# Optimization experiments

Hardware: AMD Instinct MI355X
Metric: run time of the kernel (lower is better)

The kernel has to match this reference:

```python
import jax, jax.numpy as jnp
import numpy as np

BN_EPS = 1e-5


def setup_inputs() -> dict:
    key = jax.random.key(0)
    k1, k2, k3 = jax.random.split(key, 3)
    B, C, N = 8, 64, 4096
    x = jax.random.normal(k1, (B, C, N, 1), dtype=jnp.float32)
    w = jax.random.normal(k2, (B, N), dtype=jnp.float32)
    conv_w = jax.random.normal(k3, (C, C, 1, 1), dtype=jnp.float32) * (1.0 / np.sqrt(C))
    conv_b = jnp.zeros((C,), dtype=jnp.float32)
    bn_gamma = jnp.ones((C,), dtype=jnp.float32)
    bn_beta = jnp.zeros((C,), dtype=jnp.float32)
    return {"x": x, "w": w, "conv_w": conv_w, "conv_b": conv_b,
            "bn_gamma": bn_gamma, "bn_beta": bn_beta}


def _graph_aggregation(x, w):
    # x: [B, C, N, 1], w: [B, N]
    B, C, N, _ = x.shape
    wv = jax.nn.relu(jnp.tanh(w))                       # [B, N]
    # torch.bmm(w^T, w) with w [B,N,1] -> [B,1,1] inner product (faithful)
    s = jnp.sum(wv * wv, axis=-1)[:, None, None]        # [B, 1, 1]
    A = s + jnp.eye(N, dtype=x.dtype)                   # broadcast -> [B, N, N]
    d = jnp.sum(A, axis=-1)                             # [B, N]
    dinv = (1.0 / d) ** 0.5                             # [B, N]
    # diag(D) @ A @ diag(D) == row/col scaling (same math, no diag materialize)
    L = dinv[:, :, None] * A * dinv[:, None, :]         # [B, N, N]
    L = jax.lax.stop_gradient(L)                        # torch.no_grad block
    feat = jnp.transpose(x[..., 0], (0, 2, 1))          # [B, N, C]
    out = jnp.einsum('bnm,bmc->bnc', L, feat)           # [B, N, C]
    return jnp.transpose(out, (0, 2, 1))[..., None]     # [B, C, N, 1]


def reference(x, w, conv_w, conv_b, bn_gamma, bn_beta):
    out = _graph_aggregation(x, w)                      # [B, C, N, 1]
    # 1x1 conv == channel matmul
    y = jnp.einsum('oc,bcnk->bonk', conv_w[:, :, 0, 0], out) + conv_b[None, :, None, None]
    # BatchNorm2d (training-mode forward: batch statistics over B,N,1)
    mean = jnp.mean(y, axis=(0, 2, 3), keepdims=True)
    var = jnp.var(y, axis=(0, 2, 3), keepdims=True)
    yhat = (y - mean) * jax.lax.rsqrt(var + BN_EPS)
    y = yhat * bn_gamma[None, :, None, None] + bn_beta[None, :, None, None]
    return jax.nn.relu(y)
```

## Files before the change

kernel.cpp:

```cpp
#include <hip/hip_runtime.h>
#include <math.h>

#define B_ 8
#define C_ 64
#define N_ 4096
#define NT_ 32

#define GP_OFF  0
#define CSP_OFF (NT_ * B_ * C_ * C_)
#define G_OFF   (CSP_OFF + NT_ * B_ * C_)
#define CS_OFF  (G_OFF + B_ * C_ * C_)
#define SS_OFF  (CS_OFF + B_ * C_)
#define SC_OFF  (SS_OFF + B_)
#define A_OFF   (SC_OFF + B_)
#define BB_OFF  (A_OFF + B_ * C_)

__global__ __launch_bounds__(256) void k_gram(const float* __restrict__ x,
                                              const float* __restrict__ wvec,
                                              float* __restrict__ ws) {
    const int b = blockIdx.y;
    const int t = threadIdx.x;

    __shared__ float xs[128 * 65];

    if (blockIdx.x == NT_) {
        const float4* wb = reinterpret_cast<const float4*>(wvec + (size_t)b * N_);
        float p = 0.f;
        #pragma unroll
        for (int i = 0; i < 4; ++i) {
            const float4 v = wb[t + i * 256];
            const float vv[4] = {v.x, v.y, v.z, v.w};
            #pragma unroll
            for (int j = 0; j < 4; ++j)
                if (vv[j] > 0.f) { const float th = tanhf(vv[j]); p += th * th; }
        }
        #pragma unroll
        for (int m = 32; m >= 1; m >>= 1) p += __shfl_xor(p, m);
        if ((t & 63) == 0) xs[t >> 6] = p;
        __syncthreads();
        if (t == 0) {
            const float s = xs[0] + xs[1] + xs[2] + xs[3];
            ws[SS_OFF + b] = s;
            ws[SC_OFF + b] = 1.f / ((float)N_ * s + 1.f);
        }
        return;
    }

    const int tile = blockIdx.x;
    const float* xb = x + (size_t)b * C_ * N_ + (size_t)tile * 128;

    const int k0 = (t & 31) * 4;
    float csum[8];
    #pragma unroll
    for (int it = 0; it < 8; ++it) {
        const int cc = it * 8 + (t >> 5);
        const float4 v = *reinterpret_cast<const float4*>(xb + (size_t)cc * N_ + k0);
        xs[(k0 + 0) * 65 + cc] = v.x;
        xs[(k0 + 1) * 65 + cc] = v.y;
        xs[(k0 + 2) * 65 + cc] = v.z;
        xs[(k0 + 3) * 65 + cc] = v.w;
        csum[it] = v.x + v.y + v.z + v.w;
    }
    __syncthreads();

    const int c1 = (t >> 4) * 4;
    const int c2 = (t & 15) * 4;
    float acc[4][4] = {};
    for (int k = 0; k < 128; ++k) {
        const float* row = &xs[k * 65];
        const float a0 = row[c1 + 0], a1 = row[c1 + 1], a2 = row[c1 + 2], a3 = row[c1 + 3];
        const float b0 = row[c2 + 0], b1 = row[c2 + 1], b2 = row[c2 + 2], b3 = row[c2 + 3];
        acc[0][0] += a0 * b0; acc[0][1] += a0 * b1; acc[0][2] += a0 * b2; acc[0][3] += a0 * b3;
        acc[1][0] += a1 * b0; acc[1][1] += a1 * b1; acc[1][2] += a1 * b2; acc[1][3] += a1 * b3;
        acc[2][0] += a2 * b0; acc[2][1] += a2 * b1; acc[2][2] += a2 * b2; acc[2][3] += a2 * b3;
        acc[3][0] += a3 * b0; acc[3][1] += a3 * b1; acc[3][2] += a3 * b2; acc[3][3] += a3 * b3;
    }

    #pragma unroll
    for (int it = 0; it < 8; ++it) {
        float s4 = csum[it];
        #pragma unroll
        for (int m = 16; m >= 1; m >>= 1) s4 += __shfl_xor(s4, m, 32);
        if ((t & 31) == 0)
            ws[CSP_OFF + (tile * B_ + b) * C_ + it * 8 + (t >> 5)] = s4;
    }

    float* Gp = ws + GP_OFF + (size_t)(tile * B_ + b) * (C_ * C_);
    #pragma unroll
    for (int i = 0; i < 4; ++i) {
        float4 r;
        r.x = acc[i][0]; r.y = acc[i][1]; r.z = acc[i][2]; r.w = acc[i][3];
        *reinterpret_cast<float4*>(&Gp[(c1 + i) * 64 + c2]) = r;
    }
}

__global__ __launch_bounds__(256) void k_reduce(float* __restrict__ ws) {
    const int blk = blockIdx.x;
    const int b = blk >> 3, slice = blk & 7;
    const int t = threadIdx.x;

    #pragma unroll
    for (int h = 0; h < 2; ++h) {
        const int e = h * 256 + t;
        const int c = slice * 8 + (e >> 6);
        const int cc = e & 63;
        float s = 0.f;
        #pragma unroll 8
        for (int p = 0; p < NT_; ++p)
            s += ws[GP_OFF + (size_t)(p * B_ + b) * (C_ * C_) + c * 64 + cc];
        ws[G_OFF + (size_t)b * (C_ * C_) + c * 64 + cc] = s;
    }
    if (slice == 0 && t < 64) {
        float s = 0.f;
        #pragma unroll 8
        for (int p = 0; p < NT_; ++p)
            s += ws[CSP_OFF + (p * B_ + b) * C_ + t];
        ws[CS_OFF + b * 64 + t] = s;
    }
}

__global__ __launch_bounds__(256) void k_finalize(const float* __restrict__ conv_w,
                                                  const float* __restrict__ conv_b,
                                                  const float* __restrict__ gamma,
                                                  const float* __restrict__ beta,
                                                  float* __restrict__ ws) {
    const int o = blockIdx.x;
    const int t = threadIdx.x;

    __shared__ float Wrow[64];
    __shared__ float Tq[8], Qq[8];

    if (t < 64) Wrow[t] = conv_w[o * 64 + t];
    __syncthreads();

    float pT[2], pQ[2];
    #pragma unroll
    for (int h = 0; h < 2; ++h) {
        const int r = t + h * 256;
        const int bb = r >> 6, c = r & 63;
        const float* Grow = ws + G_OFF + ((size_t)(bb * 64 + c)) * 64;
        float dot = 0.f;
        #pragma unroll 8
        for (int cc = 0; cc < 64; ++cc) dot += Wrow[cc] * Grow[cc];
        pQ[h] = Wrow[c] * dot;
        pT[h] = Wrow[c] * ws[CS_OFF + bb * 64 + c];
    }
    #pragma unroll
    for (int m = 32; m >= 1; m >>= 1) {
        pQ[0] += __shfl_xor(pQ[0], m);
        pQ[1] += __shfl_xor(pQ[1], m);
        pT[0] += __shfl_xor(pT[0], m);
        pT[1] += __shfl_xor(pT[1], m);
    }
    if ((t & 63) == 0) {
        const int wv = t >> 6;
        Tq[wv] = pT[0]; Qq[wv] = pQ[0];
        Tq[wv + 4] = pT[1]; Qq[wv + 4] = pQ[1];
    }
    __syncthreads();

    if (t == 0) {
        float Sy = 0.f, Syy = 0.f;
        float qv[8];
        #pragma unroll
        for (int b = 0; b < 8; ++b) {
            const float sS = ws[SS_OFF + b];
            const float sc = ws[SC_OFF + b];
            const float T  = sc * Tq[b];
            const float q  = sS * T + conv_b[o];
            qv[b] = q;
            Sy  += T + 4096.f * q;
            Syy += sc * sc * Qq[b] + 2.f * q * T + 4096.f * q * q;
        }
        const float mean  = Sy / 32768.f;
        const float var   = Syy / 32768.f - mean * mean;
        const float alpha = gamma[o] * rsqrtf(var + 1e-5f);
        #pragma unroll
        for (int b = 0; b < 8; ++b) {
            ws[A_OFF  + b * 64 + o] = ws[SC_OFF + b] * alpha;
            ws[BB_OFF + b * 64 + o] = (qv[b] - mean) * alpha + beta[o];
        }
    }
}

__global__ __launch_bounds__(512) void k_main(const float* __restrict__ x,
                                              const float* __restrict__ conv_w,
                                              const float* __restrict__ ws,
                                              float* __restrict__ out) {
    const int nt = blockIdx.x;
    const int b  = blockIdx.y;
    const int t  = threadIdx.x;

    __shared__ float xsm[64 * 128];

    const int n0 = nt * 128;
    const float* xb = x + (size_t)b * C_ * N_ + n0;

    const int k0 = (t & 31) * 4;
    #pragma unroll
    for (int it = 0; it < 4; ++it) {
        const int cc = it * 16 + (t >> 5);
        *reinterpret_cast<float4*>(&xsm[cc * 128 + k0]) =
            *reinterpret_cast<const float4*>(xb + (size_t)cc * N_ + k0);
    }

    const int o0 = __builtin_amdgcn_readfirstlane((t >> 6) * 8);
    const int nn = (t & 63) * 2;

    float au[8], bu[8];
    #pragma unroll
    for (int i = 0; i < 8; ++i) {
        au[i] = ws[A_OFF  + b * 64 + o0 + i];
        bu[i] = ws[BB_OFF + b * 64 + o0 + i];
    }
    __syncthreads();

    float acc[8][2] = {};
    #pragma unroll 4
    for (int c = 0; c < 64; ++c) {
        const float2 xv = *reinterpret_cast<const float2*>(&xsm[c * 128 + nn]);
        #pragma unroll
        for (int i = 0; i < 8; ++i) {
            const float wv = conv_w[(o0 + i) * 64 + c];
            acc[i][0] += wv * xv.x;
            acc[i][1] += wv * xv.y;
        }
    }

    #pragma unroll
    for (int i = 0; i < 8; ++i) {
        float2 r;
        r.x = fmaxf(acc[i][0] * au[i] + bu[i], 0.f);
        r.y = fmaxf(acc[i][1] * au[i] + bu[i], 0.f);
        *reinterpret_cast<float2*>(out + ((size_t)(b * 64 + o0 + i)) * N_ + n0 + nn) = r;
    }
}

extern "C" void kernel_launch(void* const* d_in, const int* in_sizes, int n_in,
                              void* d_out, int out_size, void* d_ws, size_t ws_size,
                              hipStream_t stream) {
    (void)in_sizes; (void)n_in; (void)out_size; (void)ws_size;
    const float* x      = (const float*)d_in[0];
    const float* w      = (const float*)d_in[1];
    const float* conv_w = (const float*)d_in[2];
    const float* conv_b = (const float*)d_in[3];
    const float* gamma  = (const float*)d_in[4];
    const float* beta   = (const float*)d_in[5];
    float* out = (float*)d_out;
    float* ws  = (float*)d_ws;

    k_gram<<<dim3(NT_ + 1, B_), 256, 0, stream>>>(x, w, ws);
    k_reduce<<<64, 256, 0, stream>>>(ws);
    k_finalize<<<64, 256, 0, stream>>>(conv_w, conv_b, gamma, beta, ws);
    k_main<<<dim3(32, B_), 512, 0, stream>>>(x, conv_w, ws, out);
}
```

Baseline: 103.3 us.

## Replace Gram-matrix statistics with direct conv output and per-tile moment sums

Instead of computing per-batch channel Gram matrices to derive BatchNorm statistics analytically, the conv output W·x is computed once, stored to workspace, and its per-channel sum and sum of squares are reduced per tile. A single-block stats kernel folds these into per-(batch,channel) scale and shift. An elementwise kernel then applies the affine transform and ReLU. This drops the Gram GEMM, its partial-sum reduction and the second read of x, and cuts four launches to three. In exchange it adds a write and re-read of a full-size intermediate tensor.

```diff
diff --git a/kernel.cpp b/kernel.cpp
--- a/kernel.cpp
+++ b/kernel.cpp
@@ -6,29 +6,29 @@
 #define N_ 4096
 #define NT_ 32
 
-#define GP_OFF  0
-#define CSP_OFF (NT_ * B_ * C_ * C_)
-#define G_OFF   (CSP_OFF + NT_ * B_ * C_)
-#define CS_OFF  (G_OFF + B_ * C_ * C_)
-#define SS_OFF  (CS_OFF + B_ * C_)
+#define M_OFF   0
+#define SMP_OFF (B_ * C_ * N_)
+#define SQP_OFF (SMP_OFF + NT_ * B_ * C_)
+#define SS_OFF  (SQP_OFF + NT_ * B_ * C_)
 #define SC_OFF  (SS_OFF + B_)
 #define A_OFF   (SC_OFF + B_)
 #define BB_OFF  (A_OFF + B_ * C_)
 
-__global__ __launch_bounds__(256) void k_gram(const float* __restrict__ x,
+__global__ __launch_bounds__(512) void k_conv(const float* __restrict__ x,
                                               const float* __restrict__ wvec,
+                                              const float* __restrict__ conv_w,
                                               float* __restrict__ ws) {
     const int b = blockIdx.y;
     const int t = threadIdx.x;
 
-    __shared__ float xs[128 * 65];
+    __shared__ float xsm[64 * 128];
 
     if (blockIdx.x == NT_) {
         const float4* wb = reinterpret_cast<const float4*>(wvec + (size_t)b * N_);
         float p = 0.f;
         #pragma unroll
-        for (int i = 0; i < 4; ++i) {
-            const float4 v = wb[t + i * 256];
+        for (int i = 0; i < 2; ++i) {
+            const float4 v = wb[t + i * 512];
             const float vv[4] = {v.x, v.y, v.z, v.w};
             #pragma unroll
             for (int j = 0; j < 4; ++j)
@@ -36,10 +36,12 @@
         }
         #pragma unroll
         for (int m = 32; m >= 1; m >>= 1) p += __shfl_xor(p, m);
-        if ((t & 63) == 0) xs[t >> 6] = p;
+        if ((t & 63) == 0) xsm[t >> 6] = p;
         __syncthreads();
         if (t == 0) {
-            const float s = xs[0] + xs[1] + xs[2] + xs[3];
+            float s = 0.f;
+            #pragma unroll
+            for (int wv2 = 0; wv2 < 8; ++wv2) s += xsm[wv2];
             ws[SS_OFF + b] = s;
             ws[SC_OFF + b] = 1.f / ((float)N_ * s + 1.f);
         }
@@ -47,153 +49,7 @@
     }
 
     const int tile = blockIdx.x;
-    const float* xb = x + (size_t)b * C_ * N_ + (size_t)tile * 128;
-
-    const int k0 = (t & 31) * 4;
-    float csum[8];
-    #pragma unroll
-    for (int it = 0; it < 8; ++it) {
-        const int cc = it * 8 + (t >> 5);
-        const float4 v = *reinterpret_cast<const float4*>(xb + (size_t)cc * N_ + k0);
-        xs[(k0 + 0) * 65 + cc] = v.x;
-        xs[(k0 + 1) * 65 + cc] = v.y;
-        xs[(k0 + 2) * 65 + cc] = v.z;
-        xs[(k0 + 3) * 65 + cc] = v.w;
-        csum[it] = v.x + v.y + v.z + v.w;
-    }
-    __syncthreads();
-
-    const int c1 = (t >> 4) * 4;
-    const int c2 = (t & 15) * 4;
-    float acc[4][4] = {};
-    for (int k = 0; k < 128; ++k) {
-        const float* row = &xs[k * 65];
-        const float a0 = row[c1 + 0], a1 = row[c1 + 1], a2 = row[c1 + 2], a3 = row[c1 + 3];
-        const float b0 = row[c2 + 0], b1 = row[c2 + 1], b2 = row[c2 + 2], b3 = row[c2 + 3];
-        acc[0][0] += a0 * b0; acc[0][1] += a0 * b1; acc[0][2] += a0 * b2; acc[0][3] += a0 * b3;
-        acc[1][0] += a1 * b0; acc[1][1] += a1 * b1; acc[1][2] += a1 * b2; acc[1][3] += a1 * b3;
-        acc[2][0] += a2 * b0; acc[2][1] += a2 * b1; acc[2][2] += a2 * b2; acc[2][3] += a2 * b3;
-        acc[3][0] += a3 * b0; acc[3][1] += a3 * b1; acc[3][2] += a3 * b2; acc[3][3] += a3 * b3;
-    }
-
-    #pragma unroll
-    for (int it = 0; it < 8; ++it) {
-        float s4 = csum[it];
-        #pragma unroll
-        for (int m = 16; m >= 1; m >>= 1) s4 += __shfl_xor(s4, m, 32);
-        if ((t & 31) == 0)
-            ws[CSP_OFF + (tile * B_ + b) * C_ + it * 8 + (t >> 5)] = s4;
-    }
-
-    float* Gp = ws + GP_OFF + (size_t)(tile * B_ + b) * (C_ * C_);
-    #pragma unroll
-    for (int i = 0; i < 4; ++i) {
-        float4 r;
-        r.x = acc[i][0]; r.y = acc[i][1]; r.z = acc[i][2]; r.w = acc[i][3];
-        *reinterpret_cast<float4*>(&Gp[(c1 + i) * 64 + c2]) = r;
-    }
-}
-
-__global__ __launch_bounds__(256) void k_reduce(float* __restrict__ ws) {
-    const int blk = blockIdx.x;
-    const int b = blk >> 3, slice = blk & 7;
-    const int t = threadIdx.x;
-
-    #pragma unroll
-    for (int h = 0; h < 2; ++h) {
-        const int e = h * 256 + t;
-        const int c = slice * 8 + (e >> 6);
-        const int cc = e & 63;
-        float s = 0.f;
-        #pragma unroll 8
-        for (int p = 0; p < NT_; ++p)
-            s += ws[GP_OFF + (size_t)(p * B_ + b) * (C_ * C_) + c * 64 + cc];
-        ws[G_OFF + (size_t)b * (C_ * C_) + c * 64 + cc] = s;
-    }
-    if (slice == 0 && t < 64) {
-        float s = 0.f;
-        #pragma unroll 8
-        for (int p = 0; p < NT_; ++p)
-            s += ws[CSP_OFF + (p * B_ + b) * C_ + t];
-        ws[CS_OFF + b * 64 + t] = s;
-    }
-}
-
-__global__ __launch_bounds__(256) void k_finalize(const float* __restrict__ conv_w,
-                                                  const float* __restrict__ conv_b,
-                                                  const float* __restrict__ gamma,
-                                                  const float* __restrict__ beta,
-                                                  float* __restrict__ ws) {
-    const int o = blockIdx.x;
-    const int t = threadIdx.x;
-
-    __shared__ float Wrow[64];
-    __shared__ float Tq[8], Qq[8];
-
-    if (t < 64) Wrow[t] = conv_w[o * 64 + t];
-    __syncthreads();
-
-    float pT[2], pQ[2];
-    #pragma unroll
-    for (int h = 0; h < 2; ++h) {
-        const int r = t + h * 256;
-        const int bb = r >> 6, c = r & 63;
-        const float* Grow = ws + G_OFF + ((size_t)(bb * 64 + c)) * 64;
-        float dot = 0.f;
-        #pragma unroll 8
-        for (int cc = 0; cc < 64; ++cc) dot += Wrow[cc] * Grow[cc];
-        pQ[h] = Wrow[c] * dot;
-        pT[h] = Wrow[c] * ws[CS_OFF + bb * 64 + c];
-    }
-    #pragma unroll
-    for (int m = 32; m >= 1; m >>= 1) {
-        pQ[0] += __shfl_xor(pQ[0], m);
-        pQ[1] += __shfl_xor(pQ[1], m);
-        pT[0] += __shfl_xor(pT[0], m);
-        pT[1] += __shfl_xor(pT[1], m);
-    }
-    if ((t & 63) == 0) {
-        const int wv = t >> 6;
-        Tq[wv] = pT[0]; Qq[wv] = pQ[0];
-        Tq[wv + 4] = pT[1]; Qq[wv + 4] = pQ[1];
-    }
-    __syncthreads();
-
-    if (t == 0) {
-        float Sy = 0.f, Syy = 0.f;
-        float qv[8];
-        #pragma unroll
-        for (int b = 0; b < 8; ++b) {
-            const float sS = ws[SS_OFF + b];
-            const float sc = ws[SC_OFF + b];
-            const float T  = sc * Tq[b];
-            const float q  = sS * T + conv_b[o];
-            qv[b] = q;
-            Sy  += T + 4096.f * q;
-            Syy += sc * sc * Qq[b] + 2.f * q * T + 4096.f * q * q;
-        }
-        const float mean  = Sy / 32768.f;
-        const float var   = Syy / 32768.f - mean * mean;
-        const float alpha = gamma[o] * rsqrtf(var + 1e-5f);
-        #pragma unroll
-        for (int b = 0; b < 8; ++b) {
-            ws[A_OFF  + b * 64 + o] = ws[SC_OFF + b] * alpha;
-            ws[BB_OFF + b * 64 + o] = (qv[b] - mean) * alpha + beta[o];
-        }
-    }
-}
-
-__global__ __launch_bounds__(512) void k_main(const float* __restrict__ x,
-                                              const float* __restrict__ conv_w,
-                                              const float* __restrict__ ws,
-                                              float* __restrict__ out) {
-    const int nt = blockIdx.x;
-    const int b  = blockIdx.y;
-    const int t  = threadIdx.x;
-
-    __shared__ float xsm[64 * 128];
-
-    const int n0 = nt * 128;
+    const int n0 = tile * 128;
     const float* xb = x + (size_t)b * C_ * N_ + n0;
 
     const int k0 = (t & 31) * 4;
@@ -203,17 +59,10 @@
         *reinterpret_cast<float4*>(&xsm[cc * 128 + k0]) =
             *reinterpret_cast<const float4*>(xb + (size_t)cc * N_ + k0);
     }
+    __syncthreads();
 
     const int o0 = __builtin_amdgcn_readfirstlane((t >> 6) * 8);
     const int nn = (t & 63) * 2;
-
-    float au[8], bu[8];
-    #pragma unroll
-    for (int i = 0; i < 8; ++i) {
-        au[i] = ws[A_OFF  + b * 64 + o0 + i];
-        bu[i] = ws[BB_OFF + b * 64 + o0 + i];
-    }
-    __syncthreads();
 
     float acc[8][2] = {};
     #pragma unroll 4
@@ -229,10 +78,78 @@
 
     #pragma unroll
     for (int i = 0; i < 8; ++i) {
-        float2 r;
-        r.x = fmaxf(acc[i][0] * au[i] + bu[i], 0.f);
-        r.y = fmaxf(acc[i][1] * au[i] + bu[i], 0.f);
-        *reinterpret_cast<float2*>(out + ((size_t)(b * 64 + o0 + i)) * N_ + n0 + nn) = r;
+        const int o = o0 + i;
+        *reinterpret_cast<float2*>(ws + M_OFF + ((size_t)(b * 64 + o)) * N_ + n0 + nn) =
+            make_float2(acc[i][0], acc[i][1]);
+        float s = acc[i][0] + acc[i][1];
+        float q = acc[i][0] * acc[i][0] + acc[i][1] * acc[i][1];
+        #pragma unroll
+        for (int m = 32; m >= 1; m >>= 1) {
+            s += __shfl_xor(s, m);
+            q += __shfl_xor(q, m);
+        }
+        if ((t & 63) == 0) {
+            ws[SMP_OFF + (tile * B_ + b) * C_ + o] = s;
+            ws[SQP_OFF + (tile * B_ + b) * C_ + o] = q;
+        }
+    }
+}
+
+__global__ __launch_bounds__(512) void k_stats(const float* __restrict__ conv_b,
+                                               const float* __restrict__ gamma,
+                                               const float* __restrict__ beta,
+                                               float* __restrict__ ws) {
+    const int t = threadIdx.x;
+    const int b = t >> 6, o = t & 63;
+
+    __shared__ float sTs[8][64], sTq[8][64];
+    __shared__ float sAl[64], sMe[64];
+
+    float SM = 0.f, SQ = 0.f;
+    #pragma unroll 8
+    for (int p = 0; p < NT_; ++p) {
+        SM += ws[SMP_OFF + (p * B_ + b) * C_ + o];
+        SQ += ws[SQP_OFF + (p * B_ + b) * C_ + o];
+    }
+    const float sS = ws[SS_OFF + b];
+    const float sc = ws[SC_OFF + b];
+    const float q  = sS * sc * SM + conv_b[o];
+    sTs[b][o] = sc * SM + 4096.f * q;
+    sTq[b][o] = sc * sc * SQ + 2.f * sc * q * SM + 4096.f * q * q;
+    __syncthreads();
+
+    if (t < 64) {
+        float Sy = 0.f, Syy = 0.f;
+        #pragma unroll
+        for (int bb2 = 0; bb2 < 8; ++bb2) { Sy += sTs[bb2][t]; Syy += sTq[bb2][t]; }
+        const float mean = Sy / 32768.f;
+        const float var  = Syy / 32768.f - mean * mean;
+        sAl[t] = gamma[t] * rsqrtf(var + 1e-5f);
+        sMe[t] = mean;
+    }
+    __syncthreads();
+
+    const float alpha = sAl[o];
+    ws[A_OFF  + b * 64 + o] = sc * alpha;
+    ws[BB_OFF + b * 64 + o] = (q - sMe[o]) * alpha + beta[o];
+}
+
+__global__ __launch_bounds__(256) void k_emit(const float* __restrict__ ws,
+                                              float* __restrict__ out) {
+    const int idx = blockIdx.x * 256 + threadIdx.x;
+    #pragma unroll
+    for (int h = 0; h < 2; ++h) {
+        const int e = idx + h * (1024 * 256);
+        const int row = e >> 10;
+        const float a  = ws[A_OFF + row];
+        const float bb = ws[BB_OFF + row];
+        const float4 m = *reinterpret_cast<const float4*>(ws + M_OFF + (size_t)e * 4);
+        float4 r;
+        r.x = fmaxf(m.x * a + bb, 0.f);
+        r.y = fmaxf(m.y * a + bb, 0.f);
+        r.z = fmaxf(m.z * a + bb, 0.f);
+        r.w = fmaxf(m.w * a + bb, 0.f);
+        *reinterpret_cast<float4*>(out + (size_t)e * 4) = r;
     }
 }
 
@@ -249,8 +166,7 @@
     float* out = (float*)d_out;
     float* ws  = (float*)d_ws;
 
-    k_gram<<<dim3(NT_ + 1, B_), 256, 0, stream>>>(x, w, ws);
-    k_reduce<<<64, 256, 0, stream>>>(ws);
-    k_finalize<<<64, 256, 0, stream>>>(conv_w, conv_b, gamma, beta, ws);
-    k_main<<<dim3(32, B_), 512, 0, stream>>>(x, conv_w, ws, out);
+    k_conv<<<dim3(NT_ + 1, B_), 512, 0, stream>>>(x, w, conv_w, ws);
+    k_stats<<<1, 512, 0, stream>>>(conv_b, gamma, beta, ws);
+    k_emit<<<1024, 256, 0, stream>>>(ws, out);
 }
```

Result: faster. 85.70 us (-17.1%).
